# Performance work log

Measured on AMD Instinct MI355X. Metric: run time of the kernel, lower is better.

Reference implementation:

```python
import jax, jax.numpy as jnp
import numpy as np

D = 256
K = 64


def setup_inputs() -> dict:
    key = jax.random.key(0)
    k1, k2, k3 = jax.random.split(key, 3)
    B, H, W = 16, 96, 96
    X = jax.random.normal(k1, (B, D, H, W), dtype=jnp.float32)
    std1 = 1.0 / float(np.sqrt(K * D))
    std2 = 1.0 / float(np.sqrt(K))
    codewords = jax.random.uniform(k2, (K, D), dtype=jnp.float32, minval=-std1, maxval=std1)
    scale = jax.random.uniform(k3, (K,), dtype=jnp.float32, minval=-std2, maxval=std2)
    return {"X": X, "codewords": codewords, "scale": scale}


def reference(X, codewords, scale):
    # X: [B, D, H, W] -> Xf: [B, N, D]
    B = X.shape[0]
    Xf = X.reshape(B, X.shape[1], -1).transpose(0, 2, 1)
    # Scaled L2 distances: SL[b,n,k] = scale[k] * ||x_bn - c_k||^2
    x2 = jnp.sum(Xf * Xf, axis=-1, keepdims=True)          # [B, N, 1]
    c2 = jnp.sum(codewords * codewords, axis=-1)            # [K]
    xc = jnp.einsum('bnd,kd->bnk', Xf, codewords)           # [B, N, K]
    SL = scale * (x2 - 2.0 * xc + c2)                       # [B, N, K]
    # Assignment weights: softmax over codewords K
    A = jax.nn.softmax(SL, axis=-1)                         # [B, N, K]
    # Aggregate residuals: E[b,k,d] = sum_n A[b,n,k] * (X[b,n,d] - C[k,d])
    E = jnp.einsum('bnk,bnd->bkd', A, Xf) - jnp.sum(A, axis=1)[:, :, None] * codewords
    return E
```

## Files before the change

### kernel.cpp

```cpp
#include <hip/hip_runtime.h>

#define NDIM  256
#define NK    64
#define NPIX  9216
#define NB    16
#define TN    64
#define NTILE 144
#define NW    48
#define TPB   3
#define GRID  (NB*NW)

typedef _Float16 half2_t __attribute__((ext_vector_type(2)));
typedef _Float16 half8_t __attribute__((ext_vector_type(8)));
typedef float    f32x4  __attribute__((ext_vector_type(4)));

__device__ __forceinline__ float fdot2(half2_t a, half2_t b, float c) {
  return __builtin_amdgcn_fdot2(a, b, c, false);
}

#define OFF_CH     0
#define OFF_C2     (NK * NDIM / 2)
#define OFF_ASUM   (OFF_C2 + NK)
#define OFF_APART  (OFF_ASUM + NB * NK)
#define OFF_X2     (OFF_APART + GRID * NK)
#define OFF_XH     (OFF_X2 + NB * NPIX)
#define XH_F       ((size_t)NB * NTILE * 32 * 64 * 8 / 2)
#define OFF_EPART  ((size_t)OFF_XH + XH_F)
#define WS_NEED    (OFF_EPART * 4 + (size_t)GRID * NK * NDIM * 2)

__global__ void c2ch_kernel(const float* __restrict__ Cw, float* __restrict__ c2,
                            _Float16* __restrict__ ChH) {
  const int k = blockIdx.x, t = threadIdx.x;
  const float4 v = *(const float4*)(Cw + k * NDIM + 4 * t);
  half2_t h0; h0.x = (_Float16)v.x; h0.y = (_Float16)v.y;
  half2_t h1; h1.x = (_Float16)v.z; h1.y = (_Float16)v.w;
  *(half2_t*)&ChH[k * NDIM + 4 * t]     = h0;
  *(half2_t*)&ChH[k * NDIM + 4 * t + 2] = h1;
  float s = v.x*v.x + v.y*v.y + v.z*v.z + v.w*v.w;
#pragma unroll
  for (int o = 32; o; o >>= 1) s += __shfl_down(s, o);
  if (t == 0) c2[k] = s;
}

__global__ __launch_bounds__(256) void convert_x(
    const float* __restrict__ X, _Float16* __restrict__ Xh,
    float* __restrict__ x2g) {
  __shared__ float red[4][TN];
  const int tid = threadIdx.x;
  const int w = tid >> 6, lane = tid & 63;
  const int b = blockIdx.x / NTILE, tile = blockIdx.x % NTILE;
  const int n0 = tile * TN;
  const float* Xg = X + (size_t)b * NDIM * NPIX + (size_t)(w * 64) * NPIX + n0 + lane;
  _Float16* dst = Xh + (size_t)(b * NTILE + tile) * (32 * 64 * 8);
  float xsq = 0.f;
#pragma unroll
  for (int g = 0; g < 8; ++g) {
    float v[8];
#pragma unroll
    for (int i = 0; i < 8; ++i) v[i] = Xg[(size_t)(g * 8 + i) * NPIX];
    half8_t hv;
#pragma unroll
    for (int i = 0; i < 8; ++i) { hv[i] = (_Float16)v[i]; xsq += v[i] * v[i]; }
    *(half8_t*)&dst[((w * 8 + g) * 64 + lane) * 8] = hv;
  }
  red[w][lane] = xsq;
  __syncthreads();
  if (tid < TN)
    x2g[b * NPIX + n0 + tid] = red[0][tid] + red[1][tid] + red[2][tid] + red[3][tid];
}

__global__ __launch_bounds__(256, 2) void encode_b(
    const _Float16* __restrict__ Xh, const float* __restrict__ x2g,
    const _Float16* __restrict__ ChH, const float* __restrict__ scale,
    const float* __restrict__ c2, void* __restrict__ Eout,
    float* __restrict__ Aout, int mode)
{
  __shared__ __align__(16) char smem[44032];
  _Float16* XbS = (_Float16*)smem;
  _Float16 (*Al)[72] = (_Float16(*)[72])(smem + 32768);
  float* redM = (float*)(smem + 32768 + 9216);
  float* redS = (float*)(smem + 32768 + 9216 + 1024);

  const int tid  = threadIdx.x;
  const int w    = __builtin_amdgcn_readfirstlane(tid >> 6);
  const int lane = tid & 63;
  const int m    = lane & 15, quad = lane >> 4;
  const int b    = blockIdx.x / NW;
  const int wid  = blockIdx.x % NW;
  const int kbase = w * 16;

  half8_t af1[8];
#pragma unroll
  for (int ks = 0; ks < 8; ++ks)
    af1[ks] = *(const half8_t*)(ChH + (kbase + m) * NDIM + ks * 32 + quad * 8);

  const float4 scv = *(const float4*)(scale + kbase + quad * 4);
  const float4 c2v = *(const float4*)(c2 + kbase + quad * 4);
  const float sc[4] = {scv.x, scv.y, scv.z, scv.w};
  const float sq[4] = {scv.x * c2v.x, scv.y * c2v.y, scv.z * c2v.z, scv.w * c2v.w};

  f32x4 acc_e[4][4];
#pragma unroll
  for (int i = 0; i < 4; ++i)
#pragma unroll
    for (int j = 0; j < 4; ++j)
      acc_e[i][j] = (f32x4){0.f, 0.f, 0.f, 0.f};
  float asum_r[4] = {0.f, 0.f, 0.f, 0.f};

  for (int tt = 0; tt < TPB; ++tt) {
    const int tile = wid + tt * NW;
    const _Float16* src = Xh + (size_t)(b * NTILE + tile) * (32 * 64 * 8);
    __syncthreads();

    half8_t stg[8];
#pragma unroll
    for (int r = 0; r < 8; ++r)
      stg[r] = *(const half8_t*)&src[(size_t)(tid + r * 256) * 8];
    float x2v[4];
#pragma unroll
    for (int nt = 0; nt < 4; ++nt)
      x2v[nt] = x2g[b * NPIX + tile * TN + nt * 16 + m];
#pragma unroll
    for (int r = 0; r < 8; ++r)
      *(half8_t*)&XbS[(tid + r * 256) * 8] = stg[r];
    __syncthreads();

    f32x4 accs[4];
#pragma unroll
    for (int nt = 0; nt < 4; ++nt) accs[nt] = (f32x4){0.f, 0.f, 0.f, 0.f};
#pragma unroll
    for (int ks = 0; ks < 8; ++ks) {
#pragma unroll
      for (int nt = 0; nt < 4; ++nt) {
        const half8_t bf = *(const half8_t*)&XbS[((ks * 4 + quad) * 64 + nt * 16 + m) * 8];
        accs[nt] = __builtin_amdgcn_mfma_f32_16x16x32_f16(af1[ks], bf, accs[nt], 0, 0, 0);
      }
    }

    float e[4][4], mw[4];
#pragma unroll
    for (int nt = 0; nt < 4; ++nt) {
      const int p = nt * 16 + m;
      float L[4];
      float mx = -3.0e38f;
#pragma unroll
      for (int r = 0; r < 4; ++r) {
        L[r] = sc[r] * x2v[nt] - 2.f * sc[r] * accs[nt][r] + sq[r];
        mx = fmaxf(mx, L[r]);
      }
      mx = fmaxf(mx, __shfl_xor(mx, 16));
      mx = fmaxf(mx, __shfl_xor(mx, 32));
      float s = 0.f;
#pragma unroll
      for (int r = 0; r < 4; ++r) { e[nt][r] = __expf(L[r] - mx); s += e[nt][r]; }
      s += __shfl_xor(s, 16);
      s += __shfl_xor(s, 32);
      mw[nt] = mx;
      if (lane < 16) { redM[w * 64 + p] = mx; redS[w * 64 + p] = s; }
    }
    __syncthreads();
#pragma unroll
    for (int nt = 0; nt < 4; ++nt) {
      const int p = nt * 16 + m;
      const float M = fmaxf(fmaxf(redM[0 * 64 + p], redM[1 * 64 + p]),
                            fmaxf(redM[2 * 64 + p], redM[3 * 64 + p]));
      const float T = redS[0 * 64 + p] * __expf(redM[0 * 64 + p] - M)
                    + redS[1 * 64 + p] * __expf(redM[1 * 64 + p] - M)
                    + redS[2 * 64 + p] * __expf(redM[2 * 64 + p] - M)
                    + redS[3 * 64 + p] * __expf(redM[3 * 64 + p] - M);
      const float norm = __expf(mw[nt] - M) / T;
#pragma unroll
      for (int r = 0; r < 4; ++r) {
        const float a = e[nt][r] * norm;
        Al[kbase + quad * 4 + r][p] = (_Float16)a;
        asum_r[r] += a;
      }
    }
    __syncthreads();

#pragma unroll
    for (int ks = 0; ks < 2; ++ks) {
      half8_t ba[4];
#pragma unroll
      for (int kt = 0; kt < 4; ++kt)
        ba[kt] = *(const half8_t*)&Al[kt * 16 + m][ks * 32 + quad * 8];
#pragma unroll
      for (int dt = 0; dt < 4; ++dt) {
        const int c = w * 8 + dt * 2 + (m >> 3);
        const int dlow = m & 7;
        half8_t xa;
#pragma unroll
        for (int j = 0; j < 8; ++j)
          xa[j] = XbS[((c * 64 + ks * 32 + quad * 8 + j)) * 8 + dlow];
#pragma unroll
        for (int kt = 0; kt < 4; ++kt)
          acc_e[dt][kt] = __builtin_amdgcn_mfma_f32_16x16x32_f16(xa, ba[kt], acc_e[dt][kt], 0, 0, 0);
      }
    }
  }

  __syncthreads();
  _Float16* Et = (_Float16*)smem;
#pragma unroll
  for (int dt = 0; dt < 4; ++dt)
#pragma unroll
    for (int kt = 0; kt < 4; ++kt)
#pragma unroll
      for (int r = 0; r < 4; ++r) {
        const int k = kt * 16 + m;
        const int d = w * 64 + dt * 16 + quad * 4 + r;
        Et[k * 264 + d] = (_Float16)acc_e[dt][kt][r];
      }
#pragma unroll
  for (int r = 0; r < 4; ++r) {
#pragma unroll
    for (int off = 1; off < 16; off <<= 1)
      asum_r[r] += __shfl_xor(asum_r[r], off);
  }
  __syncthreads();
  const int ko = tid >> 2, cq = tid & 3;
  if (mode) {
    _Float16* Ebk = (_Float16*)Eout + (size_t)blockIdx.x * (NK * NDIM);
#pragma unroll
    for (int g = 0; g < 8; ++g)
      *(half8_t*)&Ebk[ko * NDIM + cq * 64 + g * 8] =
          *(const half8_t*)&Et[ko * 264 + cq * 64 + g * 8];
    if (m == 0)
#pragma unroll
      for (int r = 0; r < 4; ++r)
        Aout[blockIdx.x * NK + kbase + quad * 4 + r] = asum_r[r];
  } else {
    float* Ebk = (float*)Eout + (size_t)b * (NK * NDIM);
#pragma unroll
    for (int g = 0; g < 64; ++g)
      atomicAdd(&Ebk[ko * NDIM + cq * 64 + g], (float)Et[ko * 264 + cq * 64 + g]);
    if (m == 0)
#pragma unroll
      for (int r = 0; r < 4; ++r)
        atomicAdd(&Aout[b * NK + kbase + quad * 4 + r], asum_r[r]);
  }
}

__global__ void asum_reduce_kernel(const float* __restrict__ Apart,
                                   float* __restrict__ asum) {
  const int i = blockIdx.x * 256 + threadIdx.x;
  const int bb = i >> 6, k = i & 63;
  float s = 0.f;
#pragma unroll 8
  for (int w = 0; w < NW; ++w) s += Apart[(bb * NW + w) * NK + k];
  asum[i] = s;
}

__global__ void finalize_partials(const _Float16* __restrict__ EpartH,
                                  const float* __restrict__ asum,
                                  const float* __restrict__ Cw,
                                  float* __restrict__ out) {
  const int g = blockIdx.x * 256 + threadIdx.x;
  const int i0 = g * 8;
  const int bb = i0 >> 14;
  const int o  = i0 & 16383;
  const int k  = o >> 8, d = i0 & 255;
  float s[8];
#pragma unroll
  for (int j = 0; j < 8; ++j) s[j] = 0.f;
  const _Float16* base = EpartH + (((size_t)bb * NW) << 14) + o;
#pragma unroll 4
  for (int w = 0; w < NW; ++w) {
    const half8_t v = *(const half8_t*)(base + ((size_t)w << 14));
#pragma unroll
    for (int j = 0; j < 8; ++j) s[j] += (float)v[j];
  }
  const float a = asum[bb * NK + k];
  const float4 c0 = *(const float4*)(Cw + k * NDIM + d);
  const float4 c1 = *(const float4*)(Cw + k * NDIM + d + 4);
  float4 r0, r1;
  r0.x = s[0] - a * c0.x; r0.y = s[1] - a * c0.y;
  r0.z = s[2] - a * c0.z; r0.w = s[3] - a * c0.w;
  r1.x = s[4] - a * c1.x; r1.y = s[5] - a * c1.y;
  r1.z = s[6] - a * c1.z; r1.w = s[7] - a * c1.w;
  *(float4*)(out + i0)     = r0;
  *(float4*)(out + i0 + 4) = r1;
}

__global__ void finalize_atomic(const float* __restrict__ E_acc,
                                const float* __restrict__ asum,
                                const float* __restrict__ Cw,
                                float* __restrict__ out) {
  const int i = blockIdx.x * 256 + threadIdx.x;
  const int d = i & 255;
  const int k = (i >> 8) & 63;
  const int bb = i >> 14;
  out[i] = E_acc[i] - asum[bb * NK + k] * Cw[k * NDIM + d];
}

extern "C" void kernel_launch(void* const* d_in, const int* in_sizes, int n_in,
                              void* d_out, int out_size, void* d_ws, size_t ws_size,
                              hipStream_t stream) {
  const float* X     = (const float*)d_in[0];
  const float* Cw    = (const float*)d_in[1];
  const float* scale = (const float*)d_in[2];
  float* out = (float*)d_out;

  float* wsf = (float*)d_ws;
  _Float16* ChH = (_Float16*)(wsf + OFF_CH);
  float* c2     = wsf + OFF_C2;
  float* asum   = wsf + OFF_ASUM;
  float* Apart  = wsf + OFF_APART;
  float* x2g    = wsf + OFF_X2;
  _Float16* Xh  = (_Float16*)(wsf + OFF_XH);

  c2ch_kernel<<<NK, 64, 0, stream>>>(Cw, c2, ChH);
  convert_x<<<NB * NTILE, 256, 0, stream>>>(X, Xh, x2g);
  if (ws_size >= WS_NEED) {
    _Float16* EpartH = (_Float16*)(wsf + OFF_EPART);
    encode_b<<<GRID, 256, 0, stream>>>(Xh, x2g, ChH, scale, c2, EpartH, Apart, 1);
    asum_reduce_kernel<<<4, 256, 0, stream>>>(Apart, asum);
    finalize_partials<<<(NB*NK*NDIM)/(256*8), 256, 0, stream>>>(EpartH, asum, Cw, out);
  } else {
    float* E_acc = (float*)(wsf + OFF_EPART);
    hipMemsetAsync(asum, 0, (size_t)(NB*NK) * sizeof(float), stream);
    hipMemsetAsync(E_acc, 0, (size_t)(NB*NK*NDIM) * sizeof(float), stream);
    encode_b<<<GRID, 256, 0, stream>>>(Xh, x2g, ChH, scale, c2, E_acc, asum, 0);
    finalize_atomic<<<(NB*NK*NDIM)/256, 256, 0, stream>>>(E_acc, asum, Cw, out);
  }
}
```

Before: 280.0 us.

## Fuse fp32-to-fp16 conversion of X into encode kernel with register prefetch pipeline

Removes the separate convert_x pass, which wrote an fp16 copy of X plus per-pixel squared norms to workspace. The encode kernel now reads fp32 X directly, converts it in registers and computes x^2 per tile, prefetching the next tile one iteration ahead. The X-operand fragments for the second GEMM are hoisted into registers before the shared buffer is overwritten. This drops an extra global write and read of X, but raises register pressure while launch bounds go from 2 to 3 blocks per CU, and the strided fp32 loads may coalesce less well.

```diff
diff --git a/kernel.cpp b/kernel.cpp
--- a/kernel.cpp
+++ b/kernel.cpp
@@ -14,19 +14,12 @@
 typedef _Float16 half8_t __attribute__((ext_vector_type(8)));
 typedef float    f32x4  __attribute__((ext_vector_type(4)));
 
-__device__ __forceinline__ float fdot2(half2_t a, half2_t b, float c) {
-  return __builtin_amdgcn_fdot2(a, b, c, false);
-}
-
 #define OFF_CH     0
 #define OFF_C2     (NK * NDIM / 2)
 #define OFF_ASUM   (OFF_C2 + NK)
 #define OFF_APART  (OFF_ASUM + NB * NK)
-#define OFF_X2     (OFF_APART + GRID * NK)
-#define OFF_XH     (OFF_X2 + NB * NPIX)
-#define XH_F       ((size_t)NB * NTILE * 32 * 64 * 8 / 2)
-#define OFF_EPART  ((size_t)OFF_XH + XH_F)
-#define WS_NEED    (OFF_EPART * 4 + (size_t)GRID * NK * NDIM * 2)
+#define OFF_EPART  (OFF_APART + GRID * NK)
+#define WS_NEED    ((size_t)OFF_EPART * 4 + (size_t)GRID * NK * NDIM * 2)
 
 __global__ void c2ch_kernel(const float* __restrict__ Cw, float* __restrict__ c2,
                             _Float16* __restrict__ ChH) {
@@ -42,44 +35,48 @@
   if (t == 0) c2[k] = s;
 }
 
-__global__ __launch_bounds__(256) void convert_x(
-    const float* __restrict__ X, _Float16* __restrict__ Xh,
-    float* __restrict__ x2g) {
-  __shared__ float red[4][TN];
-  const int tid = threadIdx.x;
-  const int w = tid >> 6, lane = tid & 63;
-  const int b = blockIdx.x / NTILE, tile = blockIdx.x % NTILE;
-  const int n0 = tile * TN;
-  const float* Xg = X + (size_t)b * NDIM * NPIX + (size_t)(w * 64) * NPIX + n0 + lane;
-  _Float16* dst = Xh + (size_t)(b * NTILE + tile) * (32 * 64 * 8);
-  float xsq = 0.f;
+struct Pk { half2_t h[32]; float xsq; };
+
+__device__ __forceinline__ void load_pack(const float* __restrict__ Xg, Pk& o) {
+  o.xsq = 0.f;
+#pragma unroll
+  for (int g = 0; g < 4; ++g) {
+    float v[16];
+#pragma unroll
+    for (int i = 0; i < 16; ++i) v[i] = Xg[(size_t)(g * 16 + i) * NPIX];
+#pragma unroll
+    for (int i = 0; i < 8; ++i) {
+      half2_t h; h.x = (_Float16)v[2*i]; h.y = (_Float16)v[2*i+1];
+      o.h[g * 8 + i] = h;
+      o.xsq += v[2*i] * v[2*i] + v[2*i+1] * v[2*i+1];
+    }
+  }
+}
+
+__device__ __forceinline__ void stage_store(_Float16* __restrict__ XbS,
+                                            float* __restrict__ red2,
+                                            const Pk& o, int w, int lane) {
 #pragma unroll
   for (int g = 0; g < 8; ++g) {
-    float v[8];
-#pragma unroll
-    for (int i = 0; i < 8; ++i) v[i] = Xg[(size_t)(g * 8 + i) * NPIX];
     half8_t hv;
 #pragma unroll
-    for (int i = 0; i < 8; ++i) { hv[i] = (_Float16)v[i]; xsq += v[i] * v[i]; }
-    *(half8_t*)&dst[((w * 8 + g) * 64 + lane) * 8] = hv;
-  }
-  red[w][lane] = xsq;
-  __syncthreads();
-  if (tid < TN)
-    x2g[b * NPIX + n0 + tid] = red[0][tid] + red[1][tid] + red[2][tid] + red[3][tid];
-}
-
-__global__ __launch_bounds__(256, 2) void encode_b(
-    const _Float16* __restrict__ Xh, const float* __restrict__ x2g,
-    const _Float16* __restrict__ ChH, const float* __restrict__ scale,
-    const float* __restrict__ c2, void* __restrict__ Eout,
-    float* __restrict__ Aout, int mode)
+    for (int i = 0; i < 4; ++i) { hv[2*i] = o.h[g*4+i].x; hv[2*i+1] = o.h[g*4+i].y; }
+    *(half8_t*)&XbS[((w * 8 + g) * 64 + lane) * 8] = hv;
+  }
+  red2[w * 64 + lane] = o.xsq;
+}
+
+__global__ __launch_bounds__(256, 3) void encode_b(
+    const float* __restrict__ X, const _Float16* __restrict__ ChH,
+    const float* __restrict__ scale, const float* __restrict__ c2,
+    void* __restrict__ Eout, float* __restrict__ Aout, int mode)
 {
-  __shared__ __align__(16) char smem[44032];
+  __shared__ __align__(16) char smem[45056];
   _Float16* XbS = (_Float16*)smem;
   _Float16 (*Al)[72] = (_Float16(*)[72])(smem + 32768);
-  float* redM = (float*)(smem + 32768 + 9216);
-  float* redS = (float*)(smem + 32768 + 9216 + 1024);
+  float* red2 = (float*)(smem + 41984);
+  float* redM = (float*)(smem + 43008);
+  float* redS = (float*)(smem + 44032);
 
   const int tid  = threadIdx.x;
   const int w    = __builtin_amdgcn_readfirstlane(tid >> 6);
@@ -87,6 +84,7 @@
   const int m    = lane & 15, quad = lane >> 4;
   const int b    = blockIdx.x / NW;
   const int wid  = blockIdx.x % NW;
+  const float* Xbase = X + (size_t)b * NDIM * NPIX + (size_t)(w * 64) * NPIX;
   const int kbase = w * 16;
 
   half8_t af1[8];
@@ -107,24 +105,13 @@
       acc_e[i][j] = (f32x4){0.f, 0.f, 0.f, 0.f};
   float asum_r[4] = {0.f, 0.f, 0.f, 0.f};
 
+  Pk pk;
+  load_pack(Xbase + (size_t)wid * TN + lane, pk);
+  stage_store(XbS, red2, pk, w, lane);
+  load_pack(Xbase + (size_t)(wid + NW) * TN + lane, pk);
+  __syncthreads();
+
   for (int tt = 0; tt < TPB; ++tt) {
-    const int tile = wid + tt * NW;
-    const _Float16* src = Xh + (size_t)(b * NTILE + tile) * (32 * 64 * 8);
-    __syncthreads();
-
-    half8_t stg[8];
-#pragma unroll
-    for (int r = 0; r < 8; ++r)
-      stg[r] = *(const half8_t*)&src[(size_t)(tid + r * 256) * 8];
-    float x2v[4];
-#pragma unroll
-    for (int nt = 0; nt < 4; ++nt)
-      x2v[nt] = x2g[b * NPIX + tile * TN + nt * 16 + m];
-#pragma unroll
-    for (int r = 0; r < 8; ++r)
-      *(half8_t*)&XbS[(tid + r * 256) * 8] = stg[r];
-    __syncthreads();
-
     f32x4 accs[4];
 #pragma unroll
     for (int nt = 0; nt < 4; ++nt) accs[nt] = (f32x4){0.f, 0.f, 0.f, 0.f};
@@ -136,16 +123,30 @@
         accs[nt] = __builtin_amdgcn_mfma_f32_16x16x32_f16(af1[ks], bf, accs[nt], 0, 0, 0);
       }
     }
+    half8_t xa[8];
+#pragma unroll
+    for (int ks = 0; ks < 2; ++ks)
+#pragma unroll
+      for (int dt = 0; dt < 4; ++dt) {
+        const int c = w * 8 + dt * 2 + (m >> 3);
+        const int dlow = m & 7;
+        half8_t v;
+#pragma unroll
+        for (int j = 0; j < 8; ++j)
+          v[j] = XbS[(c * 64 + ks * 32 + quad * 8 + j) * 8 + dlow];
+        xa[ks * 4 + dt] = v;
+      }
 
     float e[4][4], mw[4];
 #pragma unroll
     for (int nt = 0; nt < 4; ++nt) {
       const int p = nt * 16 + m;
+      const float x2p = red2[0*64+p] + red2[1*64+p] + red2[2*64+p] + red2[3*64+p];
       float L[4];
       float mx = -3.0e38f;
 #pragma unroll
       for (int r = 0; r < 4; ++r) {
-        L[r] = sc[r] * x2v[nt] - 2.f * sc[r] * accs[nt][r] + sq[r];
+        L[r] = sc[r] * x2p - 2.f * sc[r] * accs[nt][r] + sq[r];
         mx = fmaxf(mx, L[r]);
       }
       mx = fmaxf(mx, __shfl_xor(mx, 16));
@@ -159,15 +160,17 @@
       if (lane < 16) { redM[w * 64 + p] = mx; redS[w * 64 + p] = s; }
     }
     __syncthreads();
+
+    if (tt + 1 < TPB) stage_store(XbS, red2, pk, w, lane);
 #pragma unroll
     for (int nt = 0; nt < 4; ++nt) {
       const int p = nt * 16 + m;
-      const float M = fmaxf(fmaxf(redM[0 * 64 + p], redM[1 * 64 + p]),
-                            fmaxf(redM[2 * 64 + p], redM[3 * 64 + p]));
-      const float T = redS[0 * 64 + p] * __expf(redM[0 * 64 + p] - M)
-                    + redS[1 * 64 + p] * __expf(redM[1 * 64 + p] - M)
-                    + redS[2 * 64 + p] * __expf(redM[2 * 64 + p] - M)
-                    + redS[3 * 64 + p] * __expf(redM[3 * 64 + p] - M);
+      const float M = fmaxf(fmaxf(redM[0*64+p], redM[1*64+p]),
+                            fmaxf(redM[2*64+p], redM[3*64+p]));
+      const float T = redS[0*64+p] * __expf(redM[0*64+p] - M)
+                    + redS[1*64+p] * __expf(redM[1*64+p] - M)
+                    + redS[2*64+p] * __expf(redM[2*64+p] - M)
+                    + redS[3*64+p] * __expf(redM[3*64+p] - M);
       const float norm = __expf(mw[nt] - M) / T;
 #pragma unroll
       for (int r = 0; r < 4; ++r) {
@@ -176,6 +179,8 @@
         asum_r[r] += a;
       }
     }
+    if (tt + 2 < TPB)
+      load_pack(Xbase + (size_t)(wid + (tt + 2) * NW) * TN + lane, pk);
     __syncthreads();
 
 #pragma unroll
@@ -185,17 +190,11 @@
       for (int kt = 0; kt < 4; ++kt)
         ba[kt] = *(const half8_t*)&Al[kt * 16 + m][ks * 32 + quad * 8];
 #pragma unroll
-      for (int dt = 0; dt < 4; ++dt) {
-        const int c = w * 8 + dt * 2 + (m >> 3);
-        const int dlow = m & 7;
-        half8_t xa;
-#pragma unroll
-        for (int j = 0; j < 8; ++j)
-          xa[j] = XbS[((c * 64 + ks * 32 + quad * 8 + j)) * 8 + dlow];
+      for (int dt = 0; dt < 4; ++dt)
 #pragma unroll
         for (int kt = 0; kt < 4; ++kt)
-          acc_e[dt][kt] = __builtin_amdgcn_mfma_f32_16x16x32_f16(xa, ba[kt], acc_e[dt][kt], 0, 0, 0);
-      }
+          acc_e[dt][kt] = __builtin_amdgcn_mfma_f32_16x16x32_f16(
+              xa[ks * 4 + dt], ba[kt], acc_e[dt][kt], 0, 0, 0);
     }
   }
 
@@ -306,21 +305,18 @@
   float* c2     = wsf + OFF_C2;
   float* asum   = wsf + OFF_ASUM;
   float* Apart  = wsf + OFF_APART;
-  float* x2g    = wsf + OFF_X2;
-  _Float16* Xh  = (_Float16*)(wsf + OFF_XH);
 
   c2ch_kernel<<<NK, 64, 0, stream>>>(Cw, c2, ChH);
-  convert_x<<<NB * NTILE, 256, 0, stream>>>(X, Xh, x2g);
   if (ws_size >= WS_NEED) {
     _Float16* EpartH = (_Float16*)(wsf + OFF_EPART);
-    encode_b<<<GRID, 256, 0, stream>>>(Xh, x2g, ChH, scale, c2, EpartH, Apart, 1);
+    encode_b<<<GRID, 256, 0, stream>>>(X, ChH, scale, c2, EpartH, Apart, 1);
     asum_reduce_kernel<<<4, 256, 0, stream>>>(Apart, asum);
     finalize_partials<<<(NB*NK*NDIM)/(256*8), 256, 0, stream>>>(EpartH, asum, Cw, out);
   } else {
     float* E_acc = (float*)(wsf + OFF_EPART);
     hipMemsetAsync(asum, 0, (size_t)(NB*NK) * sizeof(float), stream);
     hipMemsetAsync(E_acc, 0, (size_t)(NB*NK*NDIM) * sizeof(float), stream);
-    encode_b<<<GRID, 256, 0, stream>>>(Xh, x2g, ChH, scale, c2, E_acc, asum, 0);
+    encode_b<<<GRID, 256, 0, stream>>>(X, ChH, scale, c2, E_acc, asum, 0);
     finalize_atomic<<<(NB*NK*NDIM)/256, 256, 0, stream>>>(E_acc, asum, Cw, out);
   }
 }
```

Result: slower. 369.2 us (+31.9%).
